# Optimization experiments

Hardware: AMD Instinct MI355X
Metric: run time of the kernel (lower is better)

The kernel has to match this reference:

```python
import jax, jax.numpy as jnp
import numpy as np

B = 2
M = 128
N = 128
D_EMBD = 512
N_HEADS = 8
D_HEAD = 64
S_WIN = 8
MW = M // S_WIN
NW = N // S_WIN
LEVELS = 3
S_REGION = [8, 6, 4]
S_POOL = [2, 2, 2]
THETA = 10000.0
POOLED = [(64, 64), (32, 32), (16, 16)]
RAD = THETA ** (-2.0 * jnp.arange(D_HEAD // 4, dtype=jnp.float32) / D_HEAD)


def rope(q, m_idx, n_idx):
    # 2D RoPE: first half of d_head rotated by row index, second half by col index
    m = m_idx.astype(jnp.float32)[:, None] * RAD  # (Lm, d_head//4)
    n = n_idx.astype(jnp.float32)[:, None] * RAD  # (Ln, d_head//4)
    cos_m, sin_m = jnp.cos(m)[:, None, :], jnp.sin(m)[:, None, :]
    cos_n, sin_n = jnp.cos(n)[None, :, :], jnp.sin(n)[None, :, :]
    d_half = D_HEAD // 2
    qm = q[..., :d_half].reshape(q.shape[:-1] + (d_half // 2, 2))
    qn = q[..., d_half:].reshape(q.shape[:-1] + (d_half // 2, 2))
    qm_rot = jnp.stack([cos_m * qm[..., 0] - sin_m * qm[..., 1],
                        sin_m * qm[..., 0] + cos_m * qm[..., 1]], axis=-1)
    qn_rot = jnp.stack([cos_n * qn[..., 0] - sin_n * qn[..., 1],
                        sin_n * qn[..., 0] + cos_n * qn[..., 1]], axis=-1)
    return jnp.concatenate([qm_rot.reshape(q.shape[:-1] + (d_half,)),
                            qn_rot.reshape(q.shape[:-1] + (d_half,))], axis=-1)


def extract_regions(X, cy, cx, k, pooled_mask):
    # X: (B,H,m,n,C), pooled_mask: (B,1,m,n,1). cy/cx mirror torch's in-place '+= pad'.
    b, h, m, n, c = X.shape
    pad = k // 2
    cy = cy + pad
    cx = cx + pad
    Xp = jnp.pad(X, ((0, 0), (0, 0), (pad, pad), (pad, pad), (0, 0)))
    mp = jnp.pad(pooled_mask, ((0, 0), (0, 0), (pad, pad), (pad, pad), (0, 0)))
    delta = jnp.arange(k) - k // 2
    YYg, XXg = jnp.meshgrid(cy, cx, indexing='ij')  # (Mw,Nw)
    YY = jnp.clip(YYg[..., None, None] + delta.reshape(1, 1, -1, 1), 0, m - 1)  # (Mw,Nw,k,1)
    XX = jnp.clip(XXg[..., None, None] + delta.reshape(1, 1, 1, -1), 0, n - 1)  # (Mw,Nw,1,k)
    regions = Xp[:, :, YY, XX, :]       # (B,H,Mw,Nw,k,k,C) broadcast gather
    mask_regions = mp[:, :, YY, XX, :]  # (B,1,Mw,Nw,k,k,1)
    mw, nw = YYg.shape
    regions = regions.transpose(0, 1, 2, 4, 3, 5, 6).reshape(b, h, mw * k, nw * k, c)
    mask_regions = mask_regions.reshape(mp.shape[0], 1, mw, nw, k * k, 1)
    return regions, mask_regions, YY - pad, XX - pad


def to_windows(x, s):
    # (B,h,Mw*s,Nw*s,d) -> (B,h,Mw,Nw,s*s,d)
    b, h, ms, ns, d = x.shape
    mw, nw = ms // s, ns // s
    return x.reshape(b, h, mw, s, nw, s, d).transpose(0, 1, 2, 4, 3, 5, 6).reshape(b, h, mw, nw, s * s, d)


def split_heads(x):
    b, m, n, _ = x.shape
    return x.reshape(b, m, n, N_HEADS, D_HEAD).transpose(0, 3, 1, 2, 4)


def forward(feature_map, pooled_map_0, pooled_map_1, pooled_map_2,
            pooled_mask_0, pooled_mask_1, pooled_mask_2,
            mask_q, freq_off, cy, cx, Wq, Wk, Wv, Wo):
    pooled_maps = [pooled_map_0, pooled_map_1, pooled_map_2]
    pooled_masks = [pooled_mask_0, pooled_mask_1, pooled_mask_2]
    Q = split_heads(feature_map @ Wq)           # (B,h,M,N,d)
    freq5 = freq_off[:, None]                   # (B,1,M,N,2*d_head)
    # query affine: M_grid/N_grid are identity arange gathers in the original code
    queries = Q * freq5[..., :D_HEAD] + freq5[..., D_HEAD:]
    queries = rope(queries, jnp.arange(M), jnp.arange(N))
    queries = to_windows(queries, S_WIN)        # (B,h,Mw,Nw,sw^2,d)
    mask_q5 = mask_q[:, None].astype(bool)      # (B,1,Mw,Nw,sw^2,1)

    K_list, V_list, maskK_list = [], [], []
    cy_run, cx_run = cy, cx
    for l in range(LEVELS):
        k = S_REGION[l]
        pad = k // 2
        Kl = split_heads(pooled_maps[l] @ Wk)
        Vl = split_heads(pooled_maps[l] @ Wv)
        pm5 = pooled_masks[l][:, None]          # (B,1,m,n,1)
        cy_run = cy_run // S_POOL[l]
        cx_run = cx_run // S_POOL[l]
        K_reg, mask_K, YY, XX = extract_regions(Kl, cy_run, cx_run, k, pm5)
        # torch extract_regions mutates cy/cx in place (+pad), so V sees shifted centers
        V_reg, _, _, _ = extract_regions(Vl, cy_run + pad, cx_run + pad, k, pm5)
        cy_run = cy_run + 2 * pad
        cx_run = cx_run + 2 * pad
        m_idx = jnp.clip(YY[:, 0, :, 0].reshape(-1) * S_POOL[l], 0, M - 1)  # (Mw*k,)
        n_idx = jnp.clip(XX[0, :, 0, :].reshape(-1) * S_POOL[l], 0, N - 1)  # (Nw*k,)
        fgl = freq5[:, :, m_idx[:, None], n_idx[None, :], :]  # (B,1,Mw*k,Nw*k,2d)
        K_reg = rope(K_reg * fgl[..., :D_HEAD] + fgl[..., D_HEAD:], m_idx, n_idx)
        V_reg = rope(V_reg * fgl[..., :D_HEAD] + fgl[..., D_HEAD:], m_idx, n_idx)
        K_list.append(to_windows(K_reg, k))
        V_list.append(to_windows(V_reg, k))
        maskK_list.append(mask_K)
    keys = jnp.concatenate(K_list, axis=-2)     # (B,h,Mw,Nw,S,d), S=sum(sr^2)=116
    vals = jnp.concatenate(V_list, axis=-2)
    mask_keys = jnp.concatenate(maskK_list, axis=-2)  # (B,1,Mw,Nw,S,1)
    attn_mask = mask_q5 & jnp.swapaxes(mask_keys, -1, -2).astype(bool)
    scores = jnp.einsum('bhmnqd,bhmnkd->bhmnqk', queries, keys) / jnp.sqrt(jnp.float32(D_HEAD))
    scores = jnp.where(attn_mask, scores, jnp.finfo(scores.dtype).min)
    att = jnp.einsum('bhmnqk,bhmnkd->bhmnqd', jax.nn.softmax(scores, axis=-1), vals)
    att = att.reshape(B, N_HEADS, MW, NW, S_WIN, S_WIN, D_HEAD)
    att = att.transpose(0, 2, 4, 3, 5, 1, 6).reshape(B, M, N, N_HEADS * D_HEAD)
    return att @ Wo


def setup_inputs():
    key = jax.random.key(0)
    ks = jax.random.split(key, 12)
    inp = {}
    inp['feature_map'] = jax.random.normal(ks[0], (B, M, N, D_EMBD), dtype=jnp.float32)
    for l in range(LEVELS):
        m, n = POOLED[l]
        inp['pooled_map_%d' % l] = jax.random.normal(ks[1 + l], (B, m, n, D_EMBD), dtype=jnp.float32)
        inp['pooled_mask_%d' % l] = jnp.ones((B, m, n, 1), dtype=jnp.float32)
    inp['mask_q'] = jnp.ones((B, MW, NW, S_WIN * S_WIN, 1), dtype=bool)
    inp['freq_off'] = jax.random.normal(ks[4], (B, M, N, 2 * D_HEAD), dtype=jnp.float32) * 0.1 + 1.0
    inp['cy'] = (jnp.arange(MW) * S_WIN + S_WIN // 2).astype(jnp.int32)
    inp['cx'] = (jnp.arange(NW) * S_WIN + S_WIN // 2).astype(jnp.int32)
    inp['Wq'] = jax.random.normal(ks[5], (D_EMBD, N_HEADS * D_HEAD), dtype=jnp.float32) / np.sqrt(D_EMBD)
    inp['Wk'] = jax.random.normal(ks[6], (D_EMBD, N_HEADS * D_HEAD), dtype=jnp.float32) / np.sqrt(D_EMBD)
    inp['Wv'] = jax.random.normal(ks[7], (D_EMBD, N_HEADS * D_HEAD), dtype=jnp.float32) / np.sqrt(D_EMBD)
    inp['Wo'] = jax.random.normal(ks[8], (N_HEADS * D_HEAD, D_EMBD), dtype=jnp.float32) / np.sqrt(N_HEADS * D_HEAD)
    return inp


def reference(feature_map, pooled_map_0, pooled_map_1, pooled_map_2,
              pooled_mask_0, pooled_mask_1, pooled_mask_2,
              mask_q, freq_off, cy, cx, Wq, Wk, Wv, Wo):
    return forward(feature_map, pooled_map_0, pooled_map_1, pooled_map_2,
                   pooled_mask_0, pooled_mask_1, pooled_mask_2,
                   mask_q, freq_off, cy, cx, Wq, Wk, Wv, Wo)
```

## Files before the change

kernel.cpp:

```cpp
#include <hip/hip_runtime.h>
#include <math.h>

#define BB 2
#define MM 128
#define NN 128
#define DE 512
#define NH 8
#define DH 64
#define SWIN 8
#define MWIN 16
#define NWIN 16
#define NKEY 116
#define NSLOT 128

#define NEG_MAX (-3.402823466e38f)
#define LN1E4_OVER_32 0.28782313662425575f

#define L0_BASE 0
#define L1_BASE 8192
#define L2_BASE 10240
#define NPOS_KV 10752

typedef __bf16 bf16_t;
typedef bf16_t bf16x8 __attribute__((ext_vector_type(8)));
typedef bf16_t bf16x4 __attribute__((ext_vector_type(4)));
typedef bf16_t bf16x2 __attribute__((ext_vector_type(2)));
typedef float  f32x4  __attribute__((ext_vector_type(4)));

#define GLD16(ldsdst, gsrc)                                                  \
    __builtin_amdgcn_global_load_lds(                                        \
        (const __attribute__((address_space(1))) unsigned int*)(gsrc),       \
        (__attribute__((address_space(3))) unsigned int*)(ldsdst), 16, 0, 0)

#define CV_S0 16777216
#define CV_S1 20971520
#define CV_S2 22020096
#define CV_S3 22282240
#define CV_BLOCKS 21760
__global__ __launch_bounds__(256) void prep(
    const float* __restrict__ fmap, const float* __restrict__ p0,
    const float* __restrict__ p1, const float* __restrict__ p2,
    const float* __restrict__ Wq, const float* __restrict__ Wk,
    const float* __restrict__ Wv, const float* __restrict__ Wo,
    bf16_t* __restrict__ Afm, bf16_t* __restrict__ Ap0,
    bf16_t* __restrict__ Ap1, bf16_t* __restrict__ Ap2,
    bf16_t* __restrict__ Tq, bf16_t* __restrict__ Tk,
    bf16_t* __restrict__ Tv, bf16_t* __restrict__ To,
    float2* __restrict__ ropetab) {
    __shared__ float Ws[64][65];
    const int bid = blockIdx.x;
    const int tid = threadIdx.x;
    if (bid < CV_BLOCKS) {
        const int e = (bid * 256 + tid) * 4;
        const float* src; bf16_t* dst; int off;
        if (e < CV_S0)      { src = fmap; dst = Afm; off = e; }
        else if (e < CV_S1) { src = p0;   dst = Ap0; off = e - CV_S0; }
        else if (e < CV_S2) { src = p1;   dst = Ap1; off = e - CV_S1; }
        else if (e < CV_S3) { src = p2;   dst = Ap2; off = e - CV_S2; }
        else return;
        const float4 v = *(const float4*)(src + off);
        bf16x4 o;
        o[0] = (bf16_t)v.x; o[1] = (bf16_t)v.y; o[2] = (bf16_t)v.z; o[3] = (bf16_t)v.w;
        *(bf16x4*)(dst + off) = o;
    } else if (bid < CV_BLOCKS + 256) {
        const int idx = bid - CV_BLOCKS;
        const int w = idx >> 6, tile = idx & 63;
        const float* W = (w == 0) ? Wq : (w == 1) ? Wk : (w == 2) ? Wv : Wo;
        bf16_t*      T = (w == 0) ? Tq : (w == 1) ? Tk : (w == 2) ? Tv : To;
        const int tk0 = (tile >> 3) * 64;
        const int tn0 = (tile & 7) * 64;
#pragma unroll 4
        for (int i = 0; i < 16; ++i) {
            const int e = tid + i * 256;
            Ws[e >> 6][e & 63] = W[(tk0 + (e >> 6)) * 512 + tn0 + (e & 63)];
        }
        __syncthreads();
#pragma unroll 4
        for (int i = 0; i < 16; ++i) {
            const int e = tid + i * 256;
            const int ck = e & 63, rn = e >> 6;
            T[(size_t)(tn0 + rn) * 512 + tk0 + ck] = (bf16_t)Ws[ck][rn];
        }
    } else {
#pragma unroll
        for (int i = 0; i < 8; ++i) {
            const int e = tid * 8 + i;
            const int posn = e >> 4, p = e & 15;
            const float rad = expf(-LN1E4_OVER_32 * (float)p);
            float sn, cs;
            sincosf((float)posn * rad, &sn, &cs);
            ropetab[e] = make_float2(cs, sn);
        }
    }
}

template <int MODE>
__device__ __forceinline__ void gemm_body(bf16_t* __restrict__ sA,
                                          bf16_t* __restrict__ sB,
                                          const bf16_t* __restrict__ A,
                                          const bf16_t* __restrict__ Bt,
                                          void* __restrict__ Cp,
                                          int row0, int col0,
                                          const float* __restrict__ freq) {
    const int tid  = threadIdx.x;
    const int wave = tid >> 6;
    const int lane = tid & 63;
    const int quad = lane >> 4;
    const int lr   = lane & 15;
    const int m_w  = (wave >> 1) * 64;
    const int n_w  = (wave & 1) * 64;

    const int r8  = lane >> 3;
    const int csw = ((lane & 7) ^ r8) * 8;
    const bf16_t* gA = A  + (size_t)(row0 + wave * 32 + r8) * 512 + csw;
    const bf16_t* gB = Bt + (size_t)(col0 + wave * 32 + r8) * 512 + csw;
    bf16_t* dA = sA + wave * 2048;
    bf16_t* dB = sB + wave * 2048;

    f32x4 acc[4][4];
#pragma unroll
    for (int i = 0; i < 4; ++i)
#pragma unroll
        for (int j = 0; j < 4; ++j)
#pragma unroll
            for (int r = 0; r < 4; ++r) acc[i][j][r] = 0.0f;

    const int sw = (lr & 7) << 3;

    for (int k0 = 0; k0 < 512; k0 += 64) {
#pragma unroll
        for (int it = 0; it < 4; ++it) {
            GLD16(dA + it * 512, gA + (size_t)(it * 8) * 512 + k0);
            GLD16(dB + it * 512, gB + (size_t)(it * 8) * 512 + k0);
        }
        __syncthreads();
#pragma unroll
        for (int kk = 0; kk < 64; kk += 32) {
            bf16x8 af[4], bfr[4];
#pragma unroll
            for (int i = 0; i < 4; ++i)
                af[i] = *(const bf16x8*)&sA[(m_w + i * 16 + lr) * 64 + ((kk + quad * 8) ^ sw)];
#pragma unroll
            for (int j = 0; j < 4; ++j)
                bfr[j] = *(const bf16x8*)&sB[(n_w + j * 16 + lr) * 64 + ((kk + quad * 8) ^ sw)];
#pragma unroll
            for (int i = 0; i < 4; ++i)
#pragma unroll
                for (int j = 0; j < 4; ++j)
                    acc[i][j] = __builtin_amdgcn_mfma_f32_16x16x32_bf16(
                        af[i], bfr[j], acc[i][j], 0, 0, 0);
        }
        __syncthreads();
    }

    if (MODE == 0) {
        float* C = (float*)Cp;
#pragma unroll
        for (int i = 0; i < 4; ++i) {
            const int rb = row0 + m_w + i * 16 + quad * 4;
#pragma unroll
            for (int j = 0; j < 4; ++j) {
                const int col = col0 + n_w + j * 16 + lr;
#pragma unroll
                for (int r = 0; r < 4; ++r)
                    C[(size_t)(rb + r) * 512 + col] = acc[i][j][r];
            }
        }
    } else if (MODE == 2) {
        bf16_t* C = (bf16_t*)Cp;
#pragma unroll
        for (int i = 0; i < 4; ++i) {
            const int rb = row0 + m_w + i * 16 + quad * 4;
#pragma unroll
            for (int j = 0; j < 4; ++j) {
                const int col = col0 + n_w + j * 16 + lr;
#pragma unroll
                for (int r = 0; r < 4; ++r)
                    C[(size_t)(rb + r) * 512 + col] = (bf16_t)acc[i][j][r];
            }
        }
    } else {
        bf16_t* C = (bf16_t*)Cp;
        const int mbase = (row0 >> 7) & 127;
        const float rad0 = expf(-LN1E4_OVER_32 * (float)(lr >> 1));
        const float rad1 = expf(-LN1E4_OVER_32 * (float)(8 + (lr >> 1)));
        float cs_m[2], sn_m[2];
        sincosf((float)mbase * rad0, &sn_m[0], &cs_m[0]);
        sincosf((float)mbase * rad1, &sn_m[1], &cs_m[1]);
#pragma unroll
        for (int i = 0; i < 4; ++i) {
#pragma unroll
            for (int r = 0; r < 4; ++r) {
                const int rr = m_w + i * 16 + quad * 4 + r;
                const size_t pos = (size_t)row0 + rr;
                float sn_n[2], cs_n[2];
                sincosf((float)rr * rad0, &sn_n[0], &cs_n[0]);
                sincosf((float)rr * rad1, &sn_n[1], &cs_n[1]);
                const float* fq = freq + pos * 128;
#pragma unroll
                for (int j = 0; j < 4; ++j) {
                    const int col = col0 + n_w + j * 16 + lr;
                    const int d   = j * 16 + lr;
                    const float fs = fq[d], fo = fq[64 + d];
                    const float xp = acc[i][j][r] * fs + fo;
                    const float pr = __shfl_xor(xp, 1);
                    const float cs = (j < 2) ? cs_m[j & 1] : cs_n[j & 1];
                    const float sn = (j < 2) ? sn_m[j & 1] : sn_n[j & 1];
                    const float o  = (lr & 1) ? (sn * pr + cs * xp)
                                              : (cs * xp - sn * pr);
                    C[pos * 512 + col] = (bf16_t)o;
                }
            }
        }
    }
}

__global__ __launch_bounds__(256) void gemm_all(
    const bf16_t* __restrict__ Afm, const bf16_t* __restrict__ Ap0,
    const bf16_t* __restrict__ Ap1, const bf16_t* __restrict__ Ap2,
    const bf16_t* __restrict__ Tq, const bf16_t* __restrict__ Tk,
    const bf16_t* __restrict__ Tv,
    bf16_t* __restrict__ Qbf,
    bf16_t* __restrict__ K0, bf16_t* __restrict__ V0,
    bf16_t* __restrict__ K1, bf16_t* __restrict__ V1,
    bf16_t* __restrict__ K2, bf16_t* __restrict__ V2,
    const float* __restrict__ freq) {
    __shared__ __align__(16) bf16_t sA[128 * 64];
    __shared__ __align__(16) bf16_t sB[128 * 64];
    const int t = blockIdx.x;
    if (t < 1024) {
        gemm_body<1>(sA, sB, Afm, Tq, Qbf, (t & 255) * 128, (t >> 8) * 128, freq);
    } else if (t < 1280) {
        const int u = t - 1024;
        gemm_body<2>(sA, sB, Ap0, Tk, K0, (u & 63) * 128, (u >> 6) * 128, nullptr);
    } else if (t < 1536) {
        const int u = t - 1280;
        gemm_body<2>(sA, sB, Ap0, Tv, V0, (u & 63) * 128, (u >> 6) * 128, nullptr);
    } else if (t < 1600) {
        const int u = t - 1536;
        gemm_body<2>(sA, sB, Ap1, Tk, K1, (u & 15) * 128, (u >> 4) * 128, nullptr);
    } else if (t < 1664) {
        const int u = t - 1600;
        gemm_body<2>(sA, sB, Ap1, Tv, V1, (u & 15) * 128, (u >> 4) * 128, nullptr);
    } else if (t < 1680) {
        const int u = t - 1664;
        gemm_body<2>(sA, sB, Ap2, Tk, K2, (u & 3) * 128, (u >> 2) * 128, nullptr);
    } else {
        const int u = t - 1680;
        gemm_body<2>(sA, sB, Ap2, Tv, V2, (u & 3) * 128, (u >> 2) * 128, nullptr);
    }
}

__global__ __launch_bounds__(256) void gemm_out(const bf16_t* __restrict__ A,
                                                const bf16_t* __restrict__ Bt,
                                                float* __restrict__ C) {
    __shared__ __align__(16) bf16_t sA[128 * 64];
    __shared__ __align__(16) bf16_t sB[128 * 64];
    const int t = blockIdx.x;
    gemm_body<0>(sA, sB, A, Bt, C, (t & 255) * 128, (t >> 8) * 128, nullptr);
}

__global__ __launch_bounds__(256) void rope_kv(
    const bf16_t* __restrict__ K0, const bf16_t* __restrict__ K1, const bf16_t* __restrict__ K2,
    const bf16_t* __restrict__ V0, const bf16_t* __restrict__ V1, const bf16_t* __restrict__ V2,
    const float* __restrict__ freq, const float2* __restrict__ tab,
    bf16_t* __restrict__ RK, bf16_t* __restrict__ RV) {
    const int pos = blockIdx.x;
    int l, ml, pad, rel;
    if (pos < L1_BASE)      { l = 0; ml = 64; pad = 4; rel = pos; }
    else if (pos < L2_BASE) { l = 1; ml = 32; pad = 3; rel = pos - L1_BASE; }
    else                    { l = 2; ml = 16; pad = 2; rel = pos - L2_BASE; }
    const int b  = rel / (ml * ml);
    const int yx = rel - b * ml * ml;
    const int y  = yx / ml, x = yx % ml;
    const int vy = min(y + pad, ml - 1 - pad);
    const int vx = min(x + pad, ml - 1 - pad);
    const int mi = min(2 * y, 127), ni = min(2 * x, 127);
    const bf16_t* Kl = (l == 0) ? K0 : (l == 1) ? K1 : K2;
    const bf16_t* Vl = (l == 0) ? V0 : (l == 1) ? V1 : V2;

    const int tid = threadIdx.x;
    const int h  = tid >> 5;
    const int pr = tid & 31;
    const int p  = pr & 15;
    const int d0 = (pr < 16) ? (2 * p) : (32 + 2 * p);
    const float2 t = tab[((pr < 16) ? mi : ni) * 16 + p];
    const float cs = t.x, sn = t.y;

    const size_t fb   = ((size_t)(b * 128 + mi) * 128 + ni) * 128;
    const float fs0 = freq[fb + d0],      fs1 = freq[fb + d0 + 1];
    const float fo0 = freq[fb + 64 + d0], fo1 = freq[fb + 64 + d0 + 1];
    const size_t kidx = ((size_t)(b * ml + y) * ml + x) * 512 + h * 64 + d0;
    const size_t vidx = ((size_t)(b * ml + vy) * ml + vx) * 512 + h * 64 + d0;
    const size_t oidx = (size_t)pos * 512 + h * 64 + d0;
    {
        const float x0 = (float)Kl[kidx] * fs0 + fo0;
        const float x1 = (float)Kl[kidx + 1] * fs1 + fo1;
        bf16x2 o;
        o[0] = (bf16_t)(cs * x0 - sn * x1);
        o[1] = (bf16_t)(sn * x0 + cs * x1);
        *(bf16x2*)(RK + oidx) = o;
    }
    {
        const float x0 = (float)Vl[vidx] * fs0 + fo0;
        const float x1 = (float)Vl[vidx + 1] * fs1 + fo1;
        bf16x2 o;
        o[0] = (bf16_t)(cs * x0 - sn * x1);
        o[1] = (bf16_t)(sn * x0 + cs * x1);
        *(bf16x2*)(RV + oidx) = o;
    }
}

#define SKS 72
#define SPS 136
#define SVS 134
__global__ __launch_bounds__(256, 4) void attn_mfma(
    const bf16_t* __restrict__ Qb,
    const bf16_t* __restrict__ RK, const bf16_t* __restrict__ RV,
    const float* __restrict__ pm0, const float* __restrict__ pm1, const float* __restrict__ pm2,
    const int* __restrict__ cy, const int* __restrict__ cx,
    bf16_t* __restrict__ att) {
    __shared__ __align__(16) bf16_t sK[NSLOT * SKS];
    __shared__ __align__(16) bf16_t sVt[64 * SVS];
    __shared__ int   sOff[NSLOT];
    __shared__ float sValid[NSLOT];
    bf16_t* sP = sK;

    const int tid = threadIdx.x;
    const int h  = blockIdx.x & 7;
    const int wx = (blockIdx.x >> 3) & 15;
    const int wy = (blockIdx.x >> 7) & 15;
    const int b  = blockIdx.x >> 11;

    const int wave = tid >> 6, lane = tid & 63, quad = lane >> 4, lr = lane & 15;

    const int qrow = wave * 16 + lr;
    const int mq0 = wy * 8 + (qrow >> 3), nq0 = wx * 8 + (qrow & 7);
    const bf16_t* qp = Qb + ((size_t)((b * 128 + mq0) * 128 + nq0)) * 512 + h * 64 + quad * 8;
    const bf16x8 af0 = *(const bf16x8*)qp;
    const bf16x8 af1 = *(const bf16x8*)(qp + 32);

    if (tid < NSLOT) {
        const int j = tid;
        int off = 0;
        bool valid = false;
        if (j < NKEY) {
            const int c0y = cy[wy] >> 1, c0x = cx[wx] >> 1;
            const int c1y = (c0y + 8) >> 1, c1x = (c0x + 8) >> 1;
            const int c2y = (c1y + 6) >> 1, c2x = (c1x + 6) >> 1;
            int dy, dx, cry, crx, ml, pad, lbase;
            if (j < 64)       { dy = j >> 3;           dx = j & 7;  cry = c0y; crx = c0x; ml = 64; pad = 4; lbase = L0_BASE; }
            else if (j < 100) { int u = j - 64;  dy = u / 6;  dx = u % 6; cry = c1y; crx = c1x; ml = 32; pad = 3; lbase = L1_BASE; }
            else              { int u = j - 100; dy = u >> 2; dx = u & 3; cry = c2y; crx = c2x; ml = 16; pad = 2; lbase = L2_BASE; }
            const int ky = min(cry + dy, ml - 1) - pad;
            const int kx = min(crx + dx, ml - 1) - pad;
            if (ky >= 0 && kx >= 0) {
                const float* pm = (j < 64) ? pm0 : (j < 100) ? pm1 : pm2;
                valid = (pm[(b * ml + ky) * ml + kx] != 0.0f);
            }
            off = (lbase + (b * ml + max(ky, 0)) * ml + max(kx, 0)) * 512 + h * 64;
        }
        sOff[tid]   = off;
        sValid[tid] = valid ? 1.0f : 0.0f;
    }
    __syncthreads();

#pragma unroll
    for (int it = 0; it < 4; ++it) {
        const int idx = tid + it * 256;
        const int j = idx >> 3, c = (idx & 7) * 8;
        const int off = sOff[j];
        *(bf16x8*)&sK[j * SKS + c] = *(const bf16x8*)(RK + off + c);
        const bf16x8 v = *(const bf16x8*)(RV + off + c);
#pragma unroll
        for (int e = 0; e < 8; ++e) sVt[(c + e) * SVS + j] = v[e];
    }
    __syncthreads();

    f32x4 accs[8];
#pragma unroll
    for (int nt = 0; nt < 8; ++nt)
#pragma unroll
        for (int r = 0; r < 4; ++r) accs[nt][r] = 0.0f;
#pragma unroll
    for (int nt = 0; nt < 8; ++nt) {
        const bf16x8 b0 = *(const bf16x8*)&sK[(nt * 16 + lr) * SKS + quad * 8];
        const bf16x8 b1 = *(const bf16x8*)&sK[(nt * 16 + lr) * SKS + quad * 8 + 32];
        accs[nt] = __builtin_amdgcn_mfma_f32_16x16x32_bf16(af0, b0, accs[nt], 0, 0, 0);
        accs[nt] = __builtin_amdgcn_mfma_f32_16x16x32_bf16(af1, b1, accs[nt], 0, 0, 0);
    }

    float P[8][4];
#pragma unroll
    for (int nt = 0; nt < 8; ++nt) {
        const float vf = sValid[nt * 16 + lr];
#pragma unroll
        for (int r = 0; r < 4; ++r)
            P[nt][r] = (vf != 0.0f) ? accs[nt][r] * 0.125f : NEG_MAX;
    }

#pragma unroll
    for (int r = 0; r < 4; ++r) {
        float mx = P[0][r];
#pragma unroll
        for (int nt = 1; nt < 8; ++nt) mx = fmaxf(mx, P[nt][r]);
        for (int m = 1; m < 16; m <<= 1) mx = fmaxf(mx, __shfl_xor(mx, m));
        float sum = 0.0f;
#pragma unroll
        for (int nt = 0; nt < 8; ++nt) {
            const float e = __expf(P[nt][r] - mx);
            P[nt][r] = e;
            sum += e;
        }
        for (int m = 1; m < 16; m <<= 1) sum += __shfl_xor(sum, m);
        const float inv = 1.0f / sum;
#pragma unroll
        for (int nt = 0; nt < 8; ++nt) P[nt][r] *= inv;
    }

    __syncthreads();

#pragma unroll
    for (int nt = 0; nt < 8; ++nt)
#pragma unroll
        for (int r = 0; r < 4; ++r)
            sP[(wave * 16 + quad * 4 + r) * SPS + nt * 16 + lr] = (bf16_t)P[nt][r];
    __syncthreads();

    f32x4 acco[4];
#pragma unroll
    for (int nt = 0; nt < 4; ++nt)
#pragma unroll
        for (int r = 0; r < 4; ++r) acco[nt][r] = 0.0f;

    bf16x8 pa[4];
#pragma unroll
    for (int ks = 0; ks < 4; ++ks)
        pa[ks] = *(const bf16x8*)&sP[(wave * 16 + lr) * SPS + quad * 8 + ks * 32];
#pragma unroll
    for (int nt = 0; nt < 4; ++nt) {
#pragma unroll
        for (int ks = 0; ks < 4; ++ks) {
            const bf16x8 vb = *(const bf16x8*)&sVt[(nt * 16 + lr) * SVS + quad * 8 + ks * 32];
            acco[nt] = __builtin_amdgcn_mfma_f32_16x16x32_bf16(pa[ks], vb, acco[nt], 0, 0, 0);
        }
    }

#pragma unroll
    for (int nt = 0; nt < 4; ++nt) {
#pragma unroll
        for (int r = 0; r < 4; ++r) {
            const int q  = wave * 16 + quad * 4 + r;
            const int d  = nt * 16 + lr;
            const int mq = wy * 8 + (q >> 3), nq = wx * 8 + (q & 7);
            att[((size_t)((b * 128 + mq) * 128 + nq)) * 512 + h * 64 + d] = (bf16_t)acco[nt][r];
        }
    }
}

extern "C" void kernel_launch(void* const* d_in, const int* in_sizes, int n_in,
                              void* d_out, int out_size, void* d_ws, size_t ws_size,
                              hipStream_t stream) {
    const float* fmap = (const float*)d_in[0];
    const float* p0   = (const float*)d_in[1];
    const float* pm0  = (const float*)d_in[2];
    const float* p1   = (const float*)d_in[3];
    const float* pm1  = (const float*)d_in[4];
    const float* p2   = (const float*)d_in[5];
    const float* pm2  = (const float*)d_in[6];
    const float* freq = (const float*)d_in[8];
    const int*   cy   = (const int*)d_in[9];
    const int*   cx   = (const int*)d_in[10];
    const float* Wq   = (const float*)d_in[11];
    const float* Wk   = (const float*)d_in[12];
    const float* Wv   = (const float*)d_in[13];
    const float* Wo   = (const float*)d_in[14];
    float* out = (float*)d_out;

    char* base = (char*)d_ws;
    size_t off = 0;
    auto carve = [&](size_t bytes) {
        char* p = base + off; off += (bytes + 255) & ~(size_t)255; return p;
    };
    bf16_t* Afm  = (bf16_t*)carve(33554432);
    bf16_t* Ap0  = (bf16_t*)carve(8388608);
    bf16_t* Ap1  = (bf16_t*)carve(2097152);
    bf16_t* Ap2  = (bf16_t*)carve(524288);
    bf16_t* Tq   = (bf16_t*)carve(524288);
    bf16_t* Tk   = (bf16_t*)carve(524288);
    bf16_t* Tv   = (bf16_t*)carve(524288);
    bf16_t* To   = (bf16_t*)carve(524288);
    float2* rtab = (float2*)carve(16384);
    bf16_t* Qbf  = (bf16_t*)carve(33554432);
    bf16_t* K0   = (bf16_t*)carve(8388608);
    bf16_t* V0   = (bf16_t*)carve(8388608);
    bf16_t* K1   = (bf16_t*)carve(2097152);
    bf16_t* V1   = (bf16_t*)carve(2097152);
    bf16_t* K2   = (bf16_t*)carve(524288);
    bf16_t* V2   = (bf16_t*)carve(524288);
    bf16_t* RK   = (bf16_t*)carve(11010048);
    bf16_t* RV   = (bf16_t*)carve(11010048);
    bf16_t* attb = Afm;

    prep<<<CV_BLOCKS + 257, 256, 0, stream>>>(fmap, p0, p1, p2, Wq, Wk, Wv, Wo,
                                              Afm, Ap0, Ap1, Ap2, Tq, Tk, Tv, To,
                                              rtab);

    gemm_all<<<1696, 256, 0, stream>>>(Afm, Ap0, Ap1, Ap2, Tq, Tk, Tv,
                                       Qbf, K0, V0, K1, V1, K2, V2, freq);

    rope_kv<<<NPOS_KV, 256, 0, stream>>>(K0, K1, K2, V0, V1, V2, freq, rtab, RK, RV);

    attn_mfma<<<BB * MWIN * NWIN * NH, 256, 0, stream>>>(Qbf, RK, RV,
                                                         pm0, pm1, pm2, cy, cx, attb);

    gemm_out<<<1024, 256, 0, stream>>>(attb, To, out);
}
```

Before: 296.0 us.

## Double-buffer LDS tiles in GEMM body to overlap global loads with MFMA

The shared GEMM body now uses two LDS buffers per operand and issues the next K-tile's direct-to-LDS global loads before computing on the current tile. Explicit vmcnt waits and raw s_barrier replace __syncthreads, and the K loop is fully unrolled. The goal is to hide global memory latency behind the matrix-core work in the QKV and output projections. In exchange, LDS use per block doubles to 64 KB, which may reduce occupancy, and correctness depends on the hand-written waitcnt counts matching the eight loads issued per stage.

```diff
diff --git a/kernel.cpp b/kernel.cpp
--- a/kernel.cpp
+++ b/kernel.cpp
@@ -114,8 +114,16 @@
     const int csw = ((lane & 7) ^ r8) * 8;
     const bf16_t* gA = A  + (size_t)(row0 + wave * 32 + r8) * 512 + csw;
     const bf16_t* gB = Bt + (size_t)(col0 + wave * 32 + r8) * 512 + csw;
-    bf16_t* dA = sA + wave * 2048;
-    bf16_t* dB = sB + wave * 2048;
+
+    auto stage = [&](int buf, int k0s) {
+        bf16_t* da = sA + buf * 8192 + wave * 2048;
+        bf16_t* db = sB + buf * 8192 + wave * 2048;
+#pragma unroll
+        for (int it = 0; it < 4; ++it) {
+            GLD16(da + it * 512, gA + (size_t)(it * 8) * 512 + k0s);
+            GLD16(db + it * 512, gB + (size_t)(it * 8) * 512 + k0s);
+        }
+    };
 
     f32x4 acc[4][4];
 #pragma unroll
@@ -127,22 +135,29 @@
 
     const int sw = (lr & 7) << 3;
 
+    stage(0, 0);
+#pragma unroll
     for (int k0 = 0; k0 < 512; k0 += 64) {
-#pragma unroll
-        for (int it = 0; it < 4; ++it) {
-            GLD16(dA + it * 512, gA + (size_t)(it * 8) * 512 + k0);
-            GLD16(dB + it * 512, gB + (size_t)(it * 8) * 512 + k0);
-        }
-        __syncthreads();
+        const int cur = (k0 >> 6) & 1;
+        if (k0 < 448) {
+            stage(cur ^ 1, k0 + 64);
+            asm volatile("s_waitcnt vmcnt(8)" ::: "memory");
+        } else {
+            asm volatile("s_waitcnt vmcnt(0)" ::: "memory");
+        }
+        __builtin_amdgcn_s_barrier();
+        asm volatile("" ::: "memory");
+        const bf16_t* bA = sA + cur * 8192;
+        const bf16_t* bB = sB + cur * 8192;
 #pragma unroll
         for (int kk = 0; kk < 64; kk += 32) {
             bf16x8 af[4], bfr[4];
 #pragma unroll
             for (int i = 0; i < 4; ++i)
-                af[i] = *(const bf16x8*)&sA[(m_w + i * 16 + lr) * 64 + ((kk + quad * 8) ^ sw)];
+                af[i] = *(const bf16x8*)&bA[(m_w + i * 16 + lr) * 64 + ((kk + quad * 8) ^ sw)];
 #pragma unroll
             for (int j = 0; j < 4; ++j)
-                bfr[j] = *(const bf16x8*)&sB[(n_w + j * 16 + lr) * 64 + ((kk + quad * 8) ^ sw)];
+                bfr[j] = *(const bf16x8*)&bB[(n_w + j * 16 + lr) * 64 + ((kk + quad * 8) ^ sw)];
 #pragma unroll
             for (int i = 0; i < 4; ++i)
 #pragma unroll
@@ -150,7 +165,8 @@
                     acc[i][j] = __builtin_amdgcn_mfma_f32_16x16x32_bf16(
                         af[i], bfr[j], acc[i][j], 0, 0, 0);
         }
-        __syncthreads();
+        __builtin_amdgcn_s_barrier();
+        asm volatile("" ::: "memory");
     }
 
     if (MODE == 0) {
@@ -225,8 +241,8 @@
     bf16_t* __restrict__ K1, bf16_t* __restrict__ V1,
     bf16_t* __restrict__ K2, bf16_t* __restrict__ V2,
     const float* __restrict__ freq) {
-    __shared__ __align__(16) bf16_t sA[128 * 64];
-    __shared__ __align__(16) bf16_t sB[128 * 64];
+    __shared__ __align__(16) bf16_t sA[2 * 128 * 64];
+    __shared__ __align__(16) bf16_t sB[2 * 128 * 64];
     const int t = blockIdx.x;
     if (t < 1024) {
         gemm_body<1>(sA, sB, Afm, Tq, Qbf, (t & 255) * 128, (t >> 8) * 128, freq);
@@ -254,8 +270,8 @@
 __global__ __launch_bounds__(256) void gemm_out(const bf16_t* __restrict__ A,
                                                 const bf16_t* __restrict__ Bt,
                                                 float* __restrict__ C) {
-    __shared__ __align__(16) bf16_t sA[128 * 64];
-    __shared__ __align__(16) bf16_t sB[128 * 64];
+    __shared__ __align__(16) bf16_t sA[2 * 128 * 64];
+    __shared__ __align__(16) bf16_t sB[2 * 128 * 64];
     const int t = blockIdx.x;
     gemm_body<0>(sA, sB, A, Bt, C, (t & 255) * 128, (t >> 8) * 128, nullptr);
 }
```

New measurement: 330.6 us. 1.12x slower.
